# Kernel tuning notes

Hardware: AMD Instinct MI355X
Metric: run time of the kernel (lower is better)

## Reference

```python
import jax, jax.numpy as jnp
import numpy as np

B, N, D, E, H, K = 2, 2048, 1024, 8, 2048, 2


def setup_inputs() -> dict:
    key = jax.random.key(0)
    ks = jax.random.split(key, 5)
    s = 0.02  # init scale
    return {
        "x": jax.random.normal(ks[0], (B, N, D), dtype=jnp.float32),
        "w_gate": jax.random.normal(ks[1], (D, E), dtype=jnp.float32) * s,
        "b_gate": jnp.zeros((E,), dtype=jnp.float32),
        "w1": jax.random.normal(ks[2], (E, D, H), dtype=jnp.float32) * s,
        "b1": jnp.zeros((E, H), dtype=jnp.float32),
        "w2": jax.random.normal(ks[3], (E, H, D), dtype=jnp.float32) * s,
        "b2": jnp.zeros((E, D), dtype=jnp.float32),
    }


def reference(x, w_gate, b_gate, w1, b1, w2, b2):
    b, n, d = x.shape
    T = b * n
    xf = x.reshape(T, d)                                   # (T, D)
    # --- top-k routing ---
    logits = xf @ w_gate + b_gate                          # (T, E)
    topk_logits, topk_idx = jax.lax.top_k(logits, K)       # (T, K)
    topk_gates = jax.nn.softmax(topk_logits, axis=-1)      # softmax over selected experts
    entropy = -(topk_gates * jnp.log(jnp.clip(topk_gates, 1e-8, None))).sum(-1).mean()
    # scatter top-k gates into full (T, E) gate matrix (zeros for unselected)
    gates = jnp.zeros_like(logits).at[jnp.arange(T)[:, None], topk_idx].add(topk_gates)
    # --- expert MLPs (dense over experts; gates zero out unselected) ---
    h = jax.nn.relu(jnp.einsum('td,edh->eth', xf, w1) + b1[:, None, :])  # (E, T, H)
    y = jnp.einsum('eth,ehd->etd', h, w2) + b2[:, None, :]               # (E, T, D)
    out = jnp.einsum('etd,te->td', y, gates).reshape(b, n, d)
    return out, entropy
```

## Files before the change

### kernel.cpp

```cpp
#include <hip/hip_runtime.h>

#define T_TOK 4096
#define D_DIM 1024
#define E_EXP 8
#define H_DIM 2048
#define CAP   9216
#define TILES_M 72

typedef __attribute__((ext_vector_type(8))) short bf16x8;
typedef __attribute__((ext_vector_type(4))) float f32x4;

__device__ inline unsigned short f2bf(float f) {
    unsigned int u = __float_as_uint(f);
    unsigned int r = (u + 0x7fffu + ((u >> 16) & 1u)) >> 16;
    return (unsigned short)r;
}

#define GLD_LDS16(g, l)                                                        \
    __builtin_amdgcn_global_load_lds(                                          \
        (const __attribute__((address_space(1))) void*)(g),                    \
        (__attribute__((address_space(3))) void*)(l), 16, 0, 0)

__global__ void cvt_kernel(const float* __restrict__ src,
                           unsigned short* __restrict__ dst, int n4) {
    int i = blockIdx.x * blockDim.x + threadIdx.x;
    int stride = gridDim.x * blockDim.x;
    for (; i < n4; i += stride) {
        float4 v = ((const float4*)src)[i];
        ushort4 o;
        o.x = f2bf(v.x); o.y = f2bf(v.y); o.z = f2bf(v.z); o.w = f2bf(v.w);
        ((ushort4*)dst)[i] = o;
    }
}

__global__ __launch_bounds__(256) void tcvt_kernel(const float* __restrict__ src,
                                                   unsigned short* __restrict__ dst,
                                                   int R, int C) {
    __shared__ float tile[64][65];
    size_t eo = (size_t)blockIdx.z * R * C;
    src += eo; dst += eo;
    int tx = threadIdx.x & 15, ty = threadIdx.x >> 4;
    int c0 = blockIdx.x * 64, r0 = blockIdx.y * 64;
    #pragma unroll
    for (int i = 0; i < 4; i++) {
        int row = ty + i * 16;
        float4 v = *(const float4*)&src[(size_t)(r0 + row) * C + c0 + tx * 4];
        tile[row][tx * 4 + 0] = v.x;
        tile[row][tx * 4 + 1] = v.y;
        tile[row][tx * 4 + 2] = v.z;
        tile[row][tx * 4 + 3] = v.w;
    }
    __syncthreads();
    #pragma unroll
    for (int i = 0; i < 4; i++) {
        int cc = ty + i * 16;
        int rr = tx * 4;
        ushort4 o;
        o.x = f2bf(tile[rr + 0][cc]);
        o.y = f2bf(tile[rr + 1][cc]);
        o.z = f2bf(tile[rr + 2][cc]);
        o.w = f2bf(tile[rr + 3][cc]);
        *(ushort4*)&dst[(size_t)(c0 + cc) * R + r0 + rr] = o;
    }
}

__global__ __launch_bounds__(256) void gating_kernel(
    const float* __restrict__ xf, const float* __restrict__ wg,
    const float* __restrict__ bg, int* __restrict__ tk_e,
    float* __restrict__ tk_g, float* __restrict__ ent_part)
{
    __shared__ float ents[4];
    int wave = threadIdx.x >> 6, lane = threadIdx.x & 63;
    int t = blockIdx.x * 4 + wave;
    const float* xr = xf + (size_t)t * D_DIM;
    float acc[8] = {0.f,0.f,0.f,0.f,0.f,0.f,0.f,0.f};
    for (int i = 0; i < 16; i++) {
        int d = lane + i * 64;
        float xv = xr[d];
        const float4* wr = (const float4*)(wg + (size_t)d * 8);
        float4 w0 = wr[0], w1 = wr[1];
        acc[0] += xv * w0.x; acc[1] += xv * w0.y; acc[2] += xv * w0.z; acc[3] += xv * w0.w;
        acc[4] += xv * w1.x; acc[5] += xv * w1.y; acc[6] += xv * w1.z; acc[7] += xv * w1.w;
    }
    #pragma unroll
    for (int s = 1; s < 64; s <<= 1) {
        #pragma unroll
        for (int e = 0; e < 8; e++) acc[e] += __shfl_xor(acc[e], s, 64);
    }
    if (lane == 0) {
        float l[8];
        #pragma unroll
        for (int e = 0; e < 8; e++) l[e] = acc[e] + bg[e];
        int i0 = 0;
        #pragma unroll
        for (int e = 1; e < 8; e++) if (l[e] > l[i0]) i0 = e;
        int i1 = (i0 == 0) ? 1 : 0;
        #pragma unroll
        for (int e = 0; e < 8; e++) if (e != i0 && l[e] > l[i1]) i1 = e;
        float z  = expf(l[i1] - l[i0]);
        float p0 = 1.0f / (1.0f + z);
        float p1 = z / (1.0f + z);
        float ent = -(p0 * logf(fmaxf(p0, 1e-8f)) + p1 * logf(fmaxf(p1, 1e-8f)));
        ents[wave] = ent;
        tk_e[t * 2 + 0] = i0; tk_g[t * 2 + 0] = p0;
        tk_e[t * 2 + 1] = i1; tk_g[t * 2 + 1] = p1;
    }
    __syncthreads();
    if (threadIdx.x == 0)
        ent_part[blockIdx.x] = ents[0] + ents[1] + ents[2] + ents[3];
}

__global__ __launch_bounds__(256) void ent_reduce_kernel(
    const float* __restrict__ ent_part, float* __restrict__ ent_out)
{
    __shared__ float ws_[4];
    int tid = threadIdx.x;
    float s = 0.f;
    for (int i = tid; i < T_TOK / 4; i += 256) s += ent_part[i];
    #pragma unroll
    for (int d = 1; d < 64; d <<= 1) s += __shfl_xor(s, d, 64);
    if ((tid & 63) == 0) ws_[tid >> 6] = s;
    __syncthreads();
    if (tid == 0)
        *ent_out = (ws_[0] + ws_[1] + ws_[2] + ws_[3]) * (1.0f / T_TOK);
}

__global__ __launch_bounds__(1024) void route_kernel(
    const int* __restrict__ tk_e, const float* __restrict__ tk_g,
    int* __restrict__ off, int* __restrict__ slot_token,
    float* __restrict__ slot_gate, int* __restrict__ slot_of)
{
    __shared__ int wt[16][8];
    __shared__ int wx[16][8];
    __shared__ int base[9];
    __shared__ int tot[8];

    int tid = threadIdx.x, wid = tid >> 6, lane = tid & 63;
    int i0 = tid * 8;
    int ev[8];
    *(int4*)&ev[0] = *(const int4*)&tk_e[i0];
    *(int4*)&ev[4] = *(const int4*)&tk_e[i0 + 4];

    unsigned own[4] = {0u, 0u, 0u, 0u};
    #pragma unroll
    for (int j = 0; j < 8; j++) {
        int e = ev[j];
        int reg = ((e < 4) ? 0 : 2) + (e & 1);
        own[reg] += 1u << (((e >> 1) & 1) * 16);
    }
    unsigned inc[4] = {own[0], own[1], own[2], own[3]};
    #pragma unroll
    for (int d = 1; d < 64; d <<= 1) {
        #pragma unroll
        for (int k = 0; k < 4; k++) {
            unsigned t = __shfl_up(inc[k], d, 64);
            if (lane >= d) inc[k] += t;
        }
    }
    if (lane == 63) {
        #pragma unroll
        for (int e = 0; e < 8; e++) {
            int reg = ((e < 4) ? 0 : 2) + (e & 1);
            wt[wid][e] = (inc[reg] >> (((e >> 1) & 1) * 16)) & 0xFFFF;
        }
    }
    __syncthreads();
    if (tid == 0) {
        int o = 0;
        for (int e = 0; e < 8; e++) {
            int run = 0;
            for (int w = 0; w < 16; w++) { wx[w][e] = run; run += wt[w][e]; }
            tot[e] = run;
            base[e] = o;
            off[e] = o;
            o += (run + 127) & ~127;
        }
        base[8] = o;
        off[8] = o;
    }
    __syncthreads();

    #pragma unroll
    for (int e = 0; e < 8; e++) {
        int p0 = base[e] + tot[e], p1 = base[e + 1];
        for (int i = p0 + tid; i < p1; i += 1024) slot_token[i] = -1;
    }

    unsigned run[4] = {0u, 0u, 0u, 0u};
    #pragma unroll
    for (int j = 0; j < 8; j++) {
        int e = ev[j];
        int reg = ((e < 4) ? 0 : 2) + (e & 1);
        int sh = ((e >> 1) & 1) * 16;
        int lx = (int)(((inc[reg] - own[reg]) >> sh) & 0xFFFF);
        int lr = (int)((run[reg] >> sh) & 0xFFFF);
        int slot = base[e] + wx[wid][e] + lx + lr;
        run[reg] += 1u << sh;
        int i = i0 + j;
        slot_token[slot] = i >> 1;
        slot_gate[slot] = tk_g[i];
        slot_of[i] = slot;
    }
}

__global__ __launch_bounds__(256) void gemm1_kernel(
    const unsigned short* __restrict__ xb, const unsigned short* __restrict__ w1t,
    const float* __restrict__ b1g, const int* __restrict__ off,
    const int* __restrict__ slot_token, unsigned short* __restrict__ Hb)
{
    __shared__ __align__(16) unsigned short As[128 * 32];
    __shared__ __align__(16) unsigned short Bs[128 * 32];

    int s0 = blockIdx.x * 128;
    if (s0 >= off[E_EXP]) return;
    int e = 0;
    while (s0 >= off[e + 1]) e++;
    int n0 = blockIdx.y * 128;

    int tid = threadIdx.x;
    int wave = tid >> 6, lane = tid & 63;
    int lrow = lane & 15, quad = lane >> 4;
    int srow = lane >> 2;
    int scol = (lane & 3) * 8;

    int r0 = 32 * wave + srow, r1 = r0 + 16;
    int t0 = slot_token[s0 + r0]; if (t0 < 0) t0 = 0;
    int t1 = slot_token[s0 + r1]; if (t1 < 0) t1 = 0;
    const unsigned short* a0 = xb + (size_t)t0 * D_DIM + scol;
    const unsigned short* a1 = xb + (size_t)t1 * D_DIM + scol;
    const unsigned short* wb = w1t + (size_t)e * H_DIM * D_DIM;
    const unsigned short* bp0 = wb + (size_t)(n0 + r0) * D_DIM + scol;
    const unsigned short* bp1 = wb + (size_t)(n0 + r1) * D_DIM + scol;

    unsigned short* lA0 = As + wave * 1024;
    unsigned short* lA1 = lA0 + 512;
    unsigned short* lB0 = Bs + wave * 1024;
    unsigned short* lB1 = lB0 + 512;

    f32x4 acc[4][4];
    #pragma unroll
    for (int mi = 0; mi < 4; mi++)
        #pragma unroll
        for (int ni = 0; ni < 4; ni++) acc[mi][ni] = (f32x4){0.f, 0.f, 0.f, 0.f};

    int wr = (wave >> 1) * 64, wc = (wave & 1) * 64;

    for (int k0 = 0; k0 < D_DIM; k0 += 32) {
        __syncthreads();
        GLD_LDS16(a0 + k0, lA0);
        GLD_LDS16(a1 + k0, lA1);
        GLD_LDS16(bp0 + k0, lB0);
        GLD_LDS16(bp1 + k0, lB1);
        __syncthreads();
        bf16x8 af[4], bfr[4];
        #pragma unroll
        for (int i = 0; i < 4; i++) {
            af[i]  = *(const bf16x8*)&As[(wr + i * 16 + lrow) * 32 + quad * 8];
            bfr[i] = *(const bf16x8*)&Bs[(wc + i * 16 + lrow) * 32 + quad * 8];
        }
        #pragma unroll
        for (int mi = 0; mi < 4; mi++)
            #pragma unroll
            for (int ni = 0; ni < 4; ni++)
                acc[mi][ni] = __builtin_amdgcn_mfma_f32_16x16x32_bf16(
                    af[mi], bfr[ni], acc[mi][ni], 0, 0, 0);
    }

    #pragma unroll
    for (int ni = 0; ni < 4; ni++) {
        int col = wc + ni * 16 + lrow;
        int h = n0 + col;
        float bv = b1g[e * H_DIM + h];
        #pragma unroll
        for (int mi = 0; mi < 4; mi++) {
            int mrow = wr + mi * 16 + quad * 4;
            #pragma unroll
            for (int r = 0; r < 4; r++) {
                float v = fmaxf(acc[mi][ni][r] + bv, 0.0f);
                Hb[(size_t)(s0 + mrow + r) * H_DIM + h] = f2bf(v);
            }
        }
    }
}

__global__ __launch_bounds__(256) void gemm2_kernel(
    const unsigned short* __restrict__ Hb, const unsigned short* __restrict__ w2t,
    const float* __restrict__ b2g, const int* __restrict__ off,
    unsigned short* __restrict__ Yb)
{
    __shared__ __align__(16) unsigned short As[128 * 32];
    __shared__ __align__(16) unsigned short Bs[128 * 32];

    int s0 = blockIdx.x * 128;
    if (s0 >= off[E_EXP]) return;
    int e = 0;
    while (s0 >= off[e + 1]) e++;
    int n0 = blockIdx.y * 128;

    int tid = threadIdx.x;
    int wave = tid >> 6, lane = tid & 63;
    int lrow = lane & 15, quad = lane >> 4;
    int srow = lane >> 2;
    int scol = (lane & 3) * 8;

    int r0 = 32 * wave + srow, r1 = r0 + 16;
    const unsigned short* a0 = Hb + (size_t)(s0 + r0) * H_DIM + scol;
    const unsigned short* a1 = Hb + (size_t)(s0 + r1) * H_DIM + scol;
    const unsigned short* wb = w2t + (size_t)e * D_DIM * H_DIM;
    const unsigned short* bp0 = wb + (size_t)(n0 + r0) * H_DIM + scol;
    const unsigned short* bp1 = wb + (size_t)(n0 + r1) * H_DIM + scol;

    unsigned short* lA0 = As + wave * 1024;
    unsigned short* lA1 = lA0 + 512;
    unsigned short* lB0 = Bs + wave * 1024;
    unsigned short* lB1 = lB0 + 512;

    f32x4 acc[4][4];
    #pragma unroll
    for (int mi = 0; mi < 4; mi++)
        #pragma unroll
        for (int ni = 0; ni < 4; ni++) acc[mi][ni] = (f32x4){0.f, 0.f, 0.f, 0.f};

    int wr = (wave >> 1) * 64, wc = (wave & 1) * 64;

    for (int k0 = 0; k0 < H_DIM; k0 += 32) {
        __syncthreads();
        GLD_LDS16(a0 + k0, lA0);
        GLD_LDS16(a1 + k0, lA1);
        GLD_LDS16(bp0 + k0, lB0);
        GLD_LDS16(bp1 + k0, lB1);
        __syncthreads();
        bf16x8 af[4], bfr[4];
        #pragma unroll
        for (int i = 0; i < 4; i++) {
            af[i]  = *(const bf16x8*)&As[(wr + i * 16 + lrow) * 32 + quad * 8];
            bfr[i] = *(const bf16x8*)&Bs[(wc + i * 16 + lrow) * 32 + quad * 8];
        }
        #pragma unroll
        for (int mi = 0; mi < 4; mi++)
            #pragma unroll
            for (int ni = 0; ni < 4; ni++)
                acc[mi][ni] = __builtin_amdgcn_mfma_f32_16x16x32_bf16(
                    af[mi], bfr[ni], acc[mi][ni], 0, 0, 0);
    }

    #pragma unroll
    for (int ni = 0; ni < 4; ni++) {
        int col = wc + ni * 16 + lrow;
        int d = n0 + col;
        float bv = b2g[e * D_DIM + d];
        #pragma unroll
        for (int mi = 0; mi < 4; mi++) {
            int mrow = wr + mi * 16 + quad * 4;
            #pragma unroll
            for (int r = 0; r < 4; r++) {
                Yb[(size_t)(s0 + mrow + r) * D_DIM + d] = f2bf(acc[mi][ni][r] + bv);
            }
        }
    }
}

__global__ __launch_bounds__(256) void combine_kernel(
    const unsigned short* __restrict__ Yb, const int* __restrict__ slot_of,
    const float* __restrict__ tk_g, float* __restrict__ out)
{
    int t = blockIdx.x * 2 + (threadIdx.x >> 7);
    int j = threadIdx.x & 127;
    int sA = slot_of[t * 2], sB = slot_of[t * 2 + 1];
    float gA = tk_g[t * 2], gB = tk_g[t * 2 + 1];
    uint4 va = *(const uint4*)(Yb + (size_t)sA * D_DIM + j * 8);
    uint4 vb = *(const uint4*)(Yb + (size_t)sB * D_DIM + j * 8);
    const unsigned int* pa = (const unsigned int*)&va;
    const unsigned int* pb = (const unsigned int*)&vb;
    float o[8];
    #pragma unroll
    for (int i = 0; i < 4; i++) {
        float a_lo = __uint_as_float(pa[i] << 16);
        float a_hi = __uint_as_float(pa[i] & 0xffff0000u);
        float b_lo = __uint_as_float(pb[i] << 16);
        float b_hi = __uint_as_float(pb[i] & 0xffff0000u);
        o[i * 2 + 0] = gA * a_lo + gB * b_lo;
        o[i * 2 + 1] = gA * a_hi + gB * b_hi;
    }
    float* op = out + (size_t)t * D_DIM + j * 8;
    ((float4*)op)[0] = make_float4(o[0], o[1], o[2], o[3]);
    ((float4*)op)[1] = make_float4(o[4], o[5], o[6], o[7]);
}

extern "C" void kernel_launch(void* const* d_in, const int* in_sizes, int n_in,
                              void* d_out, int out_size, void* d_ws, size_t ws_size,
                              hipStream_t stream)
{
    const float* xf = (const float*)d_in[0];
    const float* wg = (const float*)d_in[1];
    const float* bg = (const float*)d_in[2];
    const float* w1 = (const float*)d_in[3];
    const float* b1 = (const float*)d_in[4];
    const float* w2 = (const float*)d_in[5];
    const float* b2 = (const float*)d_in[6];
    float* out = (float*)d_out;

    char* p = (char*)d_ws;
    int* off    = (int*)p;
    int* tk_e   = off + 16;
    float* tk_g = (float*)(tk_e + T_TOK * 2);
    int* slot_token = (int*)(tk_g + T_TOK * 2);
    float* slot_gate = (float*)(slot_token + CAP);
    int* slot_of = (int*)(slot_gate + CAP);
    float* ent_part = (float*)(slot_of + T_TOK * 2);
    size_t ofs = ((size_t)((char*)(ent_part + T_TOK / 4) - p) + 255) & ~(size_t)255;
    unsigned short* xb  = (unsigned short*)(p + ofs); ofs += (size_t)T_TOK * D_DIM * 2;
    unsigned short* w1t = (unsigned short*)(p + ofs); ofs += (size_t)E_EXP * D_DIM * H_DIM * 2;
    unsigned short* w2t = (unsigned short*)(p + ofs); ofs += (size_t)E_EXP * H_DIM * D_DIM * 2;
    unsigned short* Hb  = (unsigned short*)(p + ofs); ofs += (size_t)CAP * H_DIM * 2;
    unsigned short* Yb  = w1t;

    cvt_kernel<<<1024, 256, 0, stream>>>(xf, xb, T_TOK * D_DIM / 4);
    tcvt_kernel<<<dim3(H_DIM / 64, D_DIM / 64, E_EXP), 256, 0, stream>>>(w1, w1t, D_DIM, H_DIM);
    tcvt_kernel<<<dim3(D_DIM / 64, H_DIM / 64, E_EXP), 256, 0, stream>>>(w2, w2t, H_DIM, D_DIM);

    gating_kernel<<<T_TOK / 4, 256, 0, stream>>>(xf, wg, bg, tk_e, tk_g, ent_part);
    ent_reduce_kernel<<<1, 256, 0, stream>>>(ent_part, out + (size_t)T_TOK * D_DIM);
    route_kernel<<<1, 1024, 0, stream>>>(tk_e, tk_g, off, slot_token, slot_gate, slot_of);
    gemm1_kernel<<<dim3(TILES_M, H_DIM / 128), 256, 0, stream>>>(xb, w1t, b1, off,
                                                                 slot_token, Hb);
    gemm2_kernel<<<dim3(TILES_M, D_DIM / 128), 256, 0, stream>>>(Hb, w2t, b2, off, Yb);
    combine_kernel<<<T_TOK / 2, 256, 0, stream>>>(Yb, slot_of, tk_g, out);
}
```

Measured before the change: 341.0 us.

## Fuse x bf16 conversion into gating and widen GEMM K-tile with swizzled LDS

Drops the separate cvt kernel: the gating kernel, which already reads x, now also writes the bf16 copy, saving one launch and one full read of x. Both expert GEMMs move from a 32-wide to a 64-wide K step, so there are half as many barrier pairs per output tile. An XOR swizzle on the LDS column groups is added to reduce bank conflicts on the fragment reads. LDS use per block doubles, which may reduce occupancy.

```diff
diff --git a/kernel.cpp b/kernel.cpp
--- a/kernel.cpp
+++ b/kernel.cpp
@@ -20,18 +20,6 @@
     __builtin_amdgcn_global_load_lds(                                          \
         (const __attribute__((address_space(1))) void*)(g),                    \
         (__attribute__((address_space(3))) void*)(l), 16, 0, 0)
-
-__global__ void cvt_kernel(const float* __restrict__ src,
-                           unsigned short* __restrict__ dst, int n4) {
-    int i = blockIdx.x * blockDim.x + threadIdx.x;
-    int stride = gridDim.x * blockDim.x;
-    for (; i < n4; i += stride) {
-        float4 v = ((const float4*)src)[i];
-        ushort4 o;
-        o.x = f2bf(v.x); o.y = f2bf(v.y); o.z = f2bf(v.z); o.w = f2bf(v.w);
-        ((ushort4*)dst)[i] = o;
-    }
-}
 
 __global__ __launch_bounds__(256) void tcvt_kernel(const float* __restrict__ src,
                                                    unsigned short* __restrict__ dst,
@@ -66,17 +54,20 @@
 
 __global__ __launch_bounds__(256) void gating_kernel(
     const float* __restrict__ xf, const float* __restrict__ wg,
-    const float* __restrict__ bg, int* __restrict__ tk_e,
-    float* __restrict__ tk_g, float* __restrict__ ent_part)
+    const float* __restrict__ bg, unsigned short* __restrict__ xb,
+    int* __restrict__ tk_e, float* __restrict__ tk_g,
+    float* __restrict__ ent_part)
 {
     __shared__ float ents[4];
     int wave = threadIdx.x >> 6, lane = threadIdx.x & 63;
     int t = blockIdx.x * 4 + wave;
     const float* xr = xf + (size_t)t * D_DIM;
+    unsigned short* xbr = xb + (size_t)t * D_DIM;
     float acc[8] = {0.f,0.f,0.f,0.f,0.f,0.f,0.f,0.f};
     for (int i = 0; i < 16; i++) {
         int d = lane + i * 64;
         float xv = xr[d];
+        xbr[d] = f2bf(xv);
         const float4* wr = (const float4*)(wg + (size_t)d * 8);
         float4 w0 = wr[0], w1 = wr[1];
         acc[0] += xv * w0.x; acc[1] += xv * w0.y; acc[2] += xv * w0.z; acc[3] += xv * w0.w;
@@ -208,8 +199,8 @@
     const float* __restrict__ b1g, const int* __restrict__ off,
     const int* __restrict__ slot_token, unsigned short* __restrict__ Hb)
 {
-    __shared__ __align__(16) unsigned short As[128 * 32];
-    __shared__ __align__(16) unsigned short Bs[128 * 32];
+    __shared__ __align__(16) unsigned short As[128 * 64];
+    __shared__ __align__(16) unsigned short Bs[128 * 64];
 
     int s0 = blockIdx.x * 128;
     if (s0 >= off[E_EXP]) return;
@@ -220,22 +211,19 @@
     int tid = threadIdx.x;
     int wave = tid >> 6, lane = tid & 63;
     int lrow = lane & 15, quad = lane >> 4;
-    int srow = lane >> 2;
-    int scol = (lane & 3) * 8;
-
-    int r0 = 32 * wave + srow, r1 = r0 + 16;
-    int t0 = slot_token[s0 + r0]; if (t0 < 0) t0 = 0;
-    int t1 = slot_token[s0 + r1]; if (t1 < 0) t1 = 0;
-    const unsigned short* a0 = xb + (size_t)t0 * D_DIM + scol;
-    const unsigned short* a1 = xb + (size_t)t1 * D_DIM + scol;
+    int srow = lane >> 3;
+    int scol = ((lane & 7) ^ srow) * 8;
+
     const unsigned short* wb = w1t + (size_t)e * H_DIM * D_DIM;
-    const unsigned short* bp0 = wb + (size_t)(n0 + r0) * D_DIM + scol;
-    const unsigned short* bp1 = wb + (size_t)(n0 + r1) * D_DIM + scol;
-
-    unsigned short* lA0 = As + wave * 1024;
-    unsigned short* lA1 = lA0 + 512;
-    unsigned short* lB0 = Bs + wave * 1024;
-    unsigned short* lB1 = lB0 + 512;
+    const unsigned short* ap[4];
+    const unsigned short* bp[4];
+    #pragma unroll
+    for (int j = 0; j < 4; j++) {
+        int r = 32 * j + 8 * wave + srow;
+        int t = slot_token[s0 + r]; if (t < 0) t = 0;
+        ap[j] = xb + (size_t)t * D_DIM + scol;
+        bp[j] = wb + (size_t)(n0 + r) * D_DIM + scol;
+    }
 
     f32x4 acc[4][4];
     #pragma unroll
@@ -244,32 +232,37 @@
         for (int ni = 0; ni < 4; ni++) acc[mi][ni] = (f32x4){0.f, 0.f, 0.f, 0.f};
 
     int wr = (wave >> 1) * 64, wc = (wave & 1) * 64;
-
-    for (int k0 = 0; k0 < D_DIM; k0 += 32) {
+    int sw = lrow & 7;
+
+    for (int k0 = 0; k0 < D_DIM; k0 += 64) {
         __syncthreads();
-        GLD_LDS16(a0 + k0, lA0);
-        GLD_LDS16(a1 + k0, lA1);
-        GLD_LDS16(bp0 + k0, lB0);
-        GLD_LDS16(bp1 + k0, lB1);
+        #pragma unroll
+        for (int j = 0; j < 4; j++) {
+            GLD_LDS16(ap[j] + k0, As + (32 * j + 8 * wave) * 64);
+            GLD_LDS16(bp[j] + k0, Bs + (32 * j + 8 * wave) * 64);
+        }
         __syncthreads();
-        bf16x8 af[4], bfr[4];
-        #pragma unroll
-        for (int i = 0; i < 4; i++) {
-            af[i]  = *(const bf16x8*)&As[(wr + i * 16 + lrow) * 32 + quad * 8];
-            bfr[i] = *(const bf16x8*)&Bs[(wc + i * 16 + lrow) * 32 + quad * 8];
-        }
-        #pragma unroll
-        for (int mi = 0; mi < 4; mi++)
-            #pragma unroll
-            for (int ni = 0; ni < 4; ni++)
-                acc[mi][ni] = __builtin_amdgcn_mfma_f32_16x16x32_bf16(
-                    af[mi], bfr[ni], acc[mi][ni], 0, 0, 0);
+        #pragma unroll
+        for (int h = 0; h < 2; h++) {
+            bf16x8 af[4], bfr[4];
+            #pragma unroll
+            for (int i = 0; i < 4; i++) {
+                int g = ((h * 4 + quad) ^ sw) * 8;
+                af[i]  = *(const bf16x8*)&As[(wr + i * 16 + lrow) * 64 + g];
+                bfr[i] = *(const bf16x8*)&Bs[(wc + i * 16 + lrow) * 64 + g];
+            }
+            #pragma unroll
+            for (int mi = 0; mi < 4; mi++)
+                #pragma unroll
+                for (int ni = 0; ni < 4; ni++)
+                    acc[mi][ni] = __builtin_amdgcn_mfma_f32_16x16x32_bf16(
+                        af[mi], bfr[ni], acc[mi][ni], 0, 0, 0);
+        }
     }
 
     #pragma unroll
     for (int ni = 0; ni < 4; ni++) {
-        int col = wc + ni * 16 + lrow;
-        int h = n0 + col;
+        int h = n0 + wc + ni * 16 + lrow;
         float bv = b1g[e * H_DIM + h];
         #pragma unroll
         for (int mi = 0; mi < 4; mi++) {
@@ -288,8 +281,8 @@
     const float* __restrict__ b2g, const int* __restrict__ off,
     unsigned short* __restrict__ Yb)
 {
-    __shared__ __align__(16) unsigned short As[128 * 32];
-    __shared__ __align__(16) unsigned short Bs[128 * 32];
+    __shared__ __align__(16) unsigned short As[128 * 64];
+    __shared__ __align__(16) unsigned short Bs[128 * 64];
 
     int s0 = blockIdx.x * 128;
     if (s0 >= off[E_EXP]) return;
@@ -300,20 +293,18 @@
     int tid = threadIdx.x;
     int wave = tid >> 6, lane = tid & 63;
     int lrow = lane & 15, quad = lane >> 4;
-    int srow = lane >> 2;
-    int scol = (lane & 3) * 8;
-
-    int r0 = 32 * wave + srow, r1 = r0 + 16;
-    const unsigned short* a0 = Hb + (size_t)(s0 + r0) * H_DIM + scol;
-    const unsigned short* a1 = Hb + (size_t)(s0 + r1) * H_DIM + scol;
+    int srow = lane >> 3;
+    int scol = ((lane & 7) ^ srow) * 8;
+
     const unsigned short* wb = w2t + (size_t)e * D_DIM * H_DIM;
-    const unsigned short* bp0 = wb + (size_t)(n0 + r0) * H_DIM + scol;
-    const unsigned short* bp1 = wb + (size_t)(n0 + r1) * H_DIM + scol;
-
-    unsigned short* lA0 = As + wave * 1024;
-    unsigned short* lA1 = lA0 + 512;
-    unsigned short* lB0 = Bs + wave * 1024;
-    unsigned short* lB1 = lB0 + 512;
+    const unsigned short* ap[4];
+    const unsigned short* bp[4];
+    #pragma unroll
+    for (int j = 0; j < 4; j++) {
+        int r = 32 * j + 8 * wave + srow;
+        ap[j] = Hb + (size_t)(s0 + r) * H_DIM + scol;
+        bp[j] = wb + (size_t)(n0 + r) * H_DIM + scol;
+    }
 
     f32x4 acc[4][4];
     #pragma unroll
@@ -322,32 +313,37 @@
         for (int ni = 0; ni < 4; ni++) acc[mi][ni] = (f32x4){0.f, 0.f, 0.f, 0.f};
 
     int wr = (wave >> 1) * 64, wc = (wave & 1) * 64;
-
-    for (int k0 = 0; k0 < H_DIM; k0 += 32) {
+    int sw = lrow & 7;
+
+    for (int k0 = 0; k0 < H_DIM; k0 += 64) {
         __syncthreads();
-        GLD_LDS16(a0 + k0, lA0);
-        GLD_LDS16(a1 + k0, lA1);
-        GLD_LDS16(bp0 + k0, lB0);
-        GLD_LDS16(bp1 + k0, lB1);
+        #pragma unroll
+        for (int j = 0; j < 4; j++) {
+            GLD_LDS16(ap[j] + k0, As + (32 * j + 8 * wave) * 64);
+            GLD_LDS16(bp[j] + k0, Bs + (32 * j + 8 * wave) * 64);
+        }
         __syncthreads();
-        bf16x8 af[4], bfr[4];
-        #pragma unroll
-        for (int i = 0; i < 4; i++) {
-            af[i]  = *(const bf16x8*)&As[(wr + i * 16 + lrow) * 32 + quad * 8];
-            bfr[i] = *(const bf16x8*)&Bs[(wc + i * 16 + lrow) * 32 + quad * 8];
-        }
-        #pragma unroll
-        for (int mi = 0; mi < 4; mi++)
-            #pragma unroll
-            for (int ni = 0; ni < 4; ni++)
-                acc[mi][ni] = __builtin_amdgcn_mfma_f32_16x16x32_bf16(
-                    af[mi], bfr[ni], acc[mi][ni], 0, 0, 0);
+        #pragma unroll
+        for (int h = 0; h < 2; h++) {
+            bf16x8 af[4], bfr[4];
+            #pragma unroll
+            for (int i = 0; i < 4; i++) {
+                int g = ((h * 4 + quad) ^ sw) * 8;
+                af[i]  = *(const bf16x8*)&As[(wr + i * 16 + lrow) * 64 + g];
+                bfr[i] = *(const bf16x8*)&Bs[(wc + i * 16 + lrow) * 64 + g];
+            }
+            #pragma unroll
+            for (int mi = 0; mi < 4; mi++)
+                #pragma unroll
+                for (int ni = 0; ni < 4; ni++)
+                    acc[mi][ni] = __builtin_amdgcn_mfma_f32_16x16x32_bf16(
+                        af[mi], bfr[ni], acc[mi][ni], 0, 0, 0);
+        }
     }
 
     #pragma unroll
     for (int ni = 0; ni < 4; ni++) {
-        int col = wc + ni * 16 + lrow;
-        int d = n0 + col;
+        int d = n0 + wc + ni * 16 + lrow;
         float bv = b2g[e * D_DIM + d];
         #pragma unroll
         for (int mi = 0; mi < 4; mi++) {
@@ -415,13 +411,11 @@
     unsigned short* Hb  = (unsigned short*)(p + ofs); ofs += (size_t)CAP * H_DIM * 2;
     unsigned short* Yb  = w1t;
 
-    cvt_kernel<<<1024, 256, 0, stream>>>(xf, xb, T_TOK * D_DIM / 4);
+    gating_kernel<<<T_TOK / 4, 256, 0, stream>>>(xf, wg, bg, xb, tk_e, tk_g, ent_part);
+    ent_reduce_kernel<<<1, 256, 0, stream>>>(ent_part, out + (size_t)T_TOK * D_DIM);
+    route_kernel<<<1, 1024, 0, stream>>>(tk_e, tk_g, off, slot_token, slot_gate, slot_of);
     tcvt_kernel<<<dim3(H_DIM / 64, D_DIM / 64, E_EXP), 256, 0, stream>>>(w1, w1t, D_DIM, H_DIM);
     tcvt_kernel<<<dim3(D_DIM / 64, H_DIM / 64, E_EXP), 256, 0, stream>>>(w2, w2t, H_DIM, D_DIM);
-
-    gating_kernel<<<T_TOK / 4, 256, 0, stream>>>(xf, wg, bg, tk_e, tk_g, ent_part);
-    ent_reduce_kernel<<<1, 256, 0, stream>>>(ent_part, out + (size_t)T_TOK * D_DIM);
-    route_kernel<<<1, 1024, 0, stream>>>(tk_e, tk_g, off, slot_token, slot_gate, slot_of);
     gemm1_kernel<<<dim3(TILES_M, H_DIM / 128), 256, 0, stream>>>(xb, w1t, b1, off,
                                                                  slot_token, Hb);
     gemm2_kernel<<<dim3(TILES_M, D_DIM / 128), 256, 0, stream>>>(Hb, w2t, b2, off, Yb);
```

Result: no change. 345.0 us (+1.2%).
